# Performance work log

Measured on AMD Instinct MI355X. Metric: run time of the kernel, lower is better.

The kernel has to match this reference:

```python
import jax, jax.numpy as jnp
import numpy as np

B = 32768
T = 1024  # num_time_bins


def setup_inputs() -> dict:
    key = jax.random.key(0)
    k1, k2, k3, k4 = jax.random.split(key, 4)
    hazard_values = jax.random.uniform(k1, (B, T), dtype=jnp.float32)
    labels_Y = jax.random.uniform(k2, (B,), dtype=jnp.float32) * T
    # nn.Linear(T, T): weight [T, T] (out, in), bias [T]
    lim = 1.0 / np.sqrt(T)
    W = jax.random.uniform(k3, (T, T), minval=-lim, maxval=lim, dtype=jnp.float32)
    b = jax.random.uniform(k4, (T,), minval=-lim, maxval=lim, dtype=jnp.float32)
    return {"hazard_values": hazard_values, "labels_Y": labels_Y, "W": W, "b": b}


def reference(hazard_values, labels_Y, W, b):
    # linear + sigmoid + argmax -> per-row truncation position
    logits = hazard_values @ W.T + b                       # [B, T]
    trunc_pos = jnp.argmax(jax.nn.sigmoid(logits), axis=1, keepdims=True)  # [B, 1] int
    # survival curve
    S = jnp.cumprod(1.0 - hazard_values, axis=1)           # [B, T]
    # vectorized truncation decay: for t >= p, multiply by exp(-(t - p))
    t = jnp.arange(T)[None, :]                             # [1, T]
    decay = jnp.where(t >= trunc_pos,
                      jnp.exp(-(t - trunc_pos).astype(S.dtype)),
                      jnp.ones((), S.dtype))
    S = S * decay
    # MSE between argmax position and labels (original prints; we skip prints)
    p = trunc_pos[:, 0].astype(jnp.float32)
    truncation_loss = jnp.mean((p - labels_Y) ** 2)
    return trunc_pos, S, truncation_loss
```

## Files before the change

kernel.cpp:

```cpp
#include <hip/hip_runtime.h>

#define B_ROWS 32768
#define T_BINS 1024

typedef __attribute__((ext_vector_type(8))) _Float16 half8;
typedef __attribute__((ext_vector_type(4))) float floatx4;

__device__ __forceinline__ unsigned long long pack_max(float v, int col) {
    unsigned x = __float_as_uint(v);
    x = (x & 0x80000000u) ? ~x : (x | 0x80000000u);
    return ((unsigned long long)x << 32) | (unsigned)(~col);
}

__device__ __forceinline__ void async16h(const _Float16* g, _Float16* l) {
    __builtin_amdgcn_global_load_lds(
        (const __attribute__((address_space(1))) unsigned int*)g,
        (__attribute__((address_space(3))) unsigned int*)l,
        16, 0, 0);
}

__global__ __launch_bounds__(256) void tof16_kernel(
    const float* __restrict__ src, _Float16* __restrict__ dst, int n4)
{
    int idx = blockIdx.x * 256 + threadIdx.x;
    if (idx >= n4) return;
    float4 x = ((const float4*)src)[idx];
    union { _Float16 h[4]; ushort4 u; } cv;
    cv.h[0] = (_Float16)x.x;
    cv.h[1] = (_Float16)x.y;
    cv.h[2] = (_Float16)x.z;
    cv.h[3] = (_Float16)x.w;
    ((ushort4*)dst)[idx] = cv.u;
}

__global__ __launch_bounds__(256, 3) void mega_kernel(
    const float* __restrict__ A, const _Float16* __restrict__ Wh,
    const float* __restrict__ bias, const float* __restrict__ labels,
    float* __restrict__ out_trunc, float* __restrict__ out_S,
    float* __restrict__ loss_acc)
{
    __shared__ _Float16 sA[2][64 * 32];
    __shared__ _Float16 sW[2][256 * 32];
    __shared__ unsigned long long cand[4][64];
    __shared__ float trunc_s[64];

    const int tid  = threadIdx.x;
    const int lane = tid & 63;
    const int wc   = tid >> 6;
    const int by   = blockIdx.x;

    const int arow  = tid >> 2;
    const int aslot = tid & 3;
    const int sAw   = arow * 32 + ((aslot ^ ((arow ^ (arow >> 2)) & 3)) * 8);
    const float* Abase = A + (size_t)(by * 64 + arow) * T_BINS + aslot * 8;

    const int l2    = lane >> 2;
    const int wksw  = ((lane & 3) ^ ((l2 ^ (l2 >> 2)) & 3)) * 8;
    const int wcol0 = wc * 64 + l2;

    const int l15   = lane & 15;
    const int hi    = lane >> 4;
    const int rslot = ((hi ^ ((l15 ^ (l15 >> 2)) & 3)) * 8);

    float run_best[4][4];
    int   run_col[4][4];
#pragma unroll
    for (int i = 0; i < 4; ++i)
#pragma unroll
        for (int r = 0; r < 4; ++r) { run_best[i][r] = -3.4e38f; run_col[i][r] = 0; }

    {
        float4 f0 = *(const float4*)(Abase);
        float4 f1 = *(const float4*)(Abase + 4);
        half8 hv;
        hv[0] = (_Float16)f0.x; hv[1] = (_Float16)f0.y;
        hv[2] = (_Float16)f0.z; hv[3] = (_Float16)f0.w;
        hv[4] = (_Float16)f1.x; hv[5] = (_Float16)f1.y;
        hv[6] = (_Float16)f1.z; hv[7] = (_Float16)f1.w;
        *(half8*)&sA[0][sAw] = hv;
    }
#pragma unroll
    for (int r = 0; r < 4; ++r)
        async16h(Wh + (size_t)(wcol0 + r * 16) * T_BINS + wksw,
                 &sW[0][wc * 2048 + r * 512]);
    float4 pa0 = *(const float4*)(Abase + 32);
    float4 pa1 = *(const float4*)(Abase + 36);
    asm volatile("s_waitcnt lgkmcnt(0)" ::: "memory");
    __builtin_amdgcn_s_barrier();

    int n = 0;
    for (int bx = 0; bx < 4; ++bx) {
        const int colbase = bx * 256 + wc * 64 + l15;
        float bj[4];
#pragma unroll
        for (int j = 0; j < 4; ++j) bj[j] = bias[colbase + j * 16];

        floatx4 acc[4][4];
#pragma unroll
        for (int i = 0; i < 4; ++i)
#pragma unroll
            for (int j = 0; j < 4; ++j) acc[i][j] = (floatx4){0.f, 0.f, 0.f, 0.f};

        for (int t = 0; t < 32; ++t, ++n) {
            const int cur = n & 1;
            const int nxt = cur ^ 1;
            const int m   = (n + 1) & 127;
            const int bxn = m >> 5;
            const int k0n = (m & 31) * 32;

            const int kq = ((n + 2) & 31) * 32;
            float4 qa0 = *(const float4*)(Abase + kq);
            float4 qa1 = *(const float4*)(Abase + kq + 4);

#pragma unroll
            for (int r = 0; r < 4; ++r)
                async16h(Wh + (size_t)(bxn * 256 + wcol0 + r * 16) * T_BINS + k0n + wksw,
                         &sW[nxt][wc * 2048 + r * 512]);

            {
                half8 hv;
                hv[0] = (_Float16)pa0.x; hv[1] = (_Float16)pa0.y;
                hv[2] = (_Float16)pa0.z; hv[3] = (_Float16)pa0.w;
                hv[4] = (_Float16)pa1.x; hv[5] = (_Float16)pa1.y;
                hv[6] = (_Float16)pa1.z; hv[7] = (_Float16)pa1.w;
                *(half8*)&sA[nxt][sAw] = hv;
            }
            pa0 = qa0; pa1 = qa1;

            asm volatile("s_waitcnt vmcnt(6)" ::: "memory");

            half8 ah[4], whf[4];
#pragma unroll
            for (int i = 0; i < 4; ++i)
                ah[i] = *(const half8*)&sA[cur][(i * 16 + l15) * 32 + rslot];
#pragma unroll
            for (int j = 0; j < 4; ++j)
                whf[j] = *(const half8*)&sW[cur][(wc * 64 + j * 16 + l15) * 32 + rslot];

            __builtin_amdgcn_s_setprio(1);
#pragma unroll
            for (int i = 0; i < 4; ++i)
#pragma unroll
                for (int j = 0; j < 4; ++j)
                    acc[i][j] = __builtin_amdgcn_mfma_f32_16x16x32_f16(ah[i], whf[j], acc[i][j], 0, 0, 0);
            __builtin_amdgcn_s_setprio(0);

            asm volatile("s_waitcnt lgkmcnt(0)" ::: "memory");
            __builtin_amdgcn_s_barrier();
        }

#pragma unroll
        for (int i = 0; i < 4; ++i)
#pragma unroll
            for (int r = 0; r < 4; ++r)
#pragma unroll
                for (int j = 0; j < 4; ++j) {
                    float v = acc[i][j][r] + bj[j];
                    if (v > run_best[i][r]) { run_best[i][r] = v; run_col[i][r] = colbase + j * 16; }
                }
    }

#pragma unroll
    for (int i = 0; i < 4; ++i)
#pragma unroll
        for (int r = 0; r < 4; ++r) {
            float best = run_best[i][r];
            int   bc   = run_col[i][r];
#pragma unroll
            for (int off = 8; off >= 1; off >>= 1) {
                float ov = __shfl_xor(best, off, 64);
                int   oc = __shfl_xor(bc, off, 64);
                if (ov > best || (ov == best && oc < bc)) { best = ov; bc = oc; }
            }
            if ((lane & 15) == 0)
                cand[wc][i * 16 + (lane >> 4) * 4 + r] = pack_max(best, bc);
        }
    __syncthreads();

    if (tid < 64) {
        unsigned long long m01 = cand[0][tid] > cand[1][tid] ? cand[0][tid] : cand[1][tid];
        unsigned long long m23 = cand[2][tid] > cand[3][tid] ? cand[2][tid] : cand[3][tid];
        unsigned long long mm = m01 > m23 ? m01 : m23;
        unsigned col = ~(unsigned)mm;
        float p = (float)col;
        int rowG = by * 64 + tid;
        out_trunc[rowG] = p;
        trunc_s[tid] = p;
        float d = p - labels[rowG];
        float term = d * d * (1.0f / (float)B_ROWS);
#pragma unroll
        for (int off = 32; off >= 1; off >>= 1)
            term += __shfl_down(term, off, 64);
        if (tid == 0) atomicAdd(loss_acc, term);
    }
    __syncthreads();

    for (int rr = 0; rr < 16; ++rr) {
        int row  = wc * 16 + rr;
        int rowG = by * 64 + row;
        const float* Hrow = A + (size_t)rowG * T_BINS + lane * 16;
        float4 h0 = *(const float4*)(Hrow + 0);
        float4 h1 = *(const float4*)(Hrow + 4);
        float4 h2 = *(const float4*)(Hrow + 8);
        float4 h3 = *(const float4*)(Hrow + 12);
        float hv[16] = {h0.x, h0.y, h0.z, h0.w, h1.x, h1.y, h1.z, h1.w,
                        h2.x, h2.y, h2.z, h2.w, h3.x, h3.y, h3.z, h3.w};
        float vprod[16];
        float run = 1.f;
#pragma unroll
        for (int j = 0; j < 16; ++j) { run *= (1.f - hv[j]); vprod[j] = run; }
        float x = run;
#pragma unroll
        for (int off = 1; off < 64; off <<= 1) {
            float o = __shfl_up(x, off, 64);
            if (lane >= off) x *= o;
        }
        float pre = __shfl_up(x, 1, 64);
        if (lane == 0) pre = 1.f;

        int p  = (int)trunc_s[row];
        int t0 = lane * 16;
        float sv[16];
#pragma unroll
        for (int j = 0; j < 16; ++j) {
            float s = pre * vprod[j];
            int t = t0 + j;
            if (t >= p) s *= __expf((float)(p - t));
            sv[j] = s;
        }
        floatx4* Srow = (floatx4*)(out_S + (size_t)rowG * T_BINS + lane * 16);
        floatx4 s0 = {sv[0],  sv[1],  sv[2],  sv[3]};
        floatx4 s1 = {sv[4],  sv[5],  sv[6],  sv[7]};
        floatx4 s2 = {sv[8],  sv[9],  sv[10], sv[11]};
        floatx4 s3 = {sv[12], sv[13], sv[14], sv[15]};
        __builtin_nontemporal_store(s0, Srow + 0);
        __builtin_nontemporal_store(s1, Srow + 1);
        __builtin_nontemporal_store(s2, Srow + 2);
        __builtin_nontemporal_store(s3, Srow + 3);
    }
}

#define BMf 64
#define BKf 16
#define LDSS (BMf + 4)
__global__ __launch_bounds__(256) void gemm_argmax_fp32(
    const float* __restrict__ A, const float* __restrict__ W,
    const float* __restrict__ bias, unsigned long long* __restrict__ rec)
{
    __shared__ float As[BKf][LDSS];
    __shared__ float Ws[BKf][LDSS];
    const int tid = threadIdx.x;
    const int tx = tid & 15, ty = tid >> 4;
    const int bx = blockIdx.x, by = blockIdx.y;
    const int ar = tid >> 2, ak = (tid & 3) << 2;
    const float* Arow = A + (size_t)(by * BMf + ar) * T_BINS + ak;
    const float* Wrow = W + (size_t)(bx * BMf + ar) * T_BINS + ak;
    float acc[4][4];
#pragma unroll
    for (int i = 0; i < 4; ++i)
#pragma unroll
        for (int j = 0; j < 4; ++j) acc[i][j] = 0.f;
    for (int k0 = 0; k0 < T_BINS; k0 += BKf) {
        float4 av = *(const float4*)(Arow + k0);
        float4 wvv = *(const float4*)(Wrow + k0);
        As[ak + 0][ar] = av.x; As[ak + 1][ar] = av.y; As[ak + 2][ar] = av.z; As[ak + 3][ar] = av.w;
        Ws[ak + 0][ar] = wvv.x; Ws[ak + 1][ar] = wvv.y; Ws[ak + 2][ar] = wvv.z; Ws[ak + 3][ar] = wvv.w;
        __syncthreads();
#pragma unroll
        for (int k = 0; k < BKf; ++k) {
            float4 a4 = *(const float4*)&As[k][ty * 4];
            float4 w4 = *(const float4*)&Ws[k][tx * 4];
            float aa[4] = {a4.x, a4.y, a4.z, a4.w};
            float ww[4] = {w4.x, w4.y, w4.z, w4.w};
#pragma unroll
            for (int i = 0; i < 4; ++i)
#pragma unroll
                for (int j = 0; j < 4; ++j) acc[i][j] = fmaf(aa[i], ww[j], acc[i][j]);
        }
        __syncthreads();
    }
    const int colBase = bx * BMf + tx * 4;
    float bv[4];
#pragma unroll
    for (int j = 0; j < 4; ++j) bv[j] = bias[colBase + j];
#pragma unroll
    for (int i = 0; i < 4; ++i) {
        float best = acc[i][0] + bv[0];
        int bc = colBase;
#pragma unroll
        for (int j = 1; j < 4; ++j) {
            float v = acc[i][j] + bv[j];
            if (v > best) { best = v; bc = colBase + j; }
        }
#pragma unroll
        for (int off = 8; off >= 1; off >>= 1) {
            float ov = __shfl_xor(best, off, 64);
            int oc = __shfl_xor(bc, off, 64);
            if (ov > best || (ov == best && oc < bc)) { best = ov; bc = oc; }
        }
        if (tx == 0) atomicMax(&rec[by * BMf + ty * 4 + i], pack_max(best, bc));
    }
}

__global__ __launch_bounds__(256) void finalize_kernel(
    const unsigned long long* __restrict__ rec, const float* __restrict__ labels,
    float* __restrict__ out_trunc, float* __restrict__ loss_acc)
{
    int i = blockIdx.x * 256 + threadIdx.x;
    unsigned col = ~(unsigned)(rec[i] & 0xFFFFFFFFull);
    float p = (float)col;
    out_trunc[i] = p;
    float d = p - labels[i];
    float term = d * d * (1.0f / (float)B_ROWS);
#pragma unroll
    for (int off = 32; off >= 1; off >>= 1)
        term += __shfl_down(term, off, 64);
    __shared__ float partials[4];
    int lane = threadIdx.x & 63, wv = threadIdx.x >> 6;
    if (lane == 0) partials[wv] = term;
    __syncthreads();
    if (threadIdx.x == 0)
        atomicAdd(loss_acc, partials[0] + partials[1] + partials[2] + partials[3]);
}

__global__ __launch_bounds__(256) void scan_kernel_f32(
    const float* __restrict__ H, const float* __restrict__ trunc_f,
    float* __restrict__ Sout)
{
    const int row = blockIdx.x;
    const int tid = threadIdx.x;
    const int lane = tid & 63;
    const int wv = tid >> 6;
    const float4 h = *(const float4*)(H + (size_t)row * T_BINS + tid * 4);
    float l0 = 1.f - h.x;
    float l1 = l0 * (1.f - h.y);
    float l2 = l1 * (1.f - h.z);
    float l3 = l2 * (1.f - h.w);
    float x = l3;
#pragma unroll
    for (int off = 1; off < 64; off <<= 1) {
        float o = __shfl_up(x, off, 64);
        if (lane >= off) x *= o;
    }
    float ex = __shfl_up(x, 1, 64);
    if (lane == 0) ex = 1.f;
    __shared__ float wtot[4];
    if (lane == 63) wtot[wv] = x;
    __syncthreads();
    float wpre = 1.f;
#pragma unroll
    for (int w = 0; w < 3; ++w)
        if (w < wv) wpre *= wtot[w];
    float pre = wpre * ex;
    int p = (int)trunc_f[row];
    int t0 = tid * 4;
    float sv[4] = {pre * l0, pre * l1, pre * l2, pre * l3};
#pragma unroll
    for (int j = 0; j < 4; ++j) {
        int t = t0 + j;
        if (t >= p) sv[j] *= __expf((float)(p - t));
    }
    float4 s4 = {sv[0], sv[1], sv[2], sv[3]};
    *(float4*)(Sout + (size_t)row * T_BINS + tid * 4) = s4;
}

extern "C" void kernel_launch(void* const* d_in, const int* in_sizes, int n_in,
                              void* d_out, int out_size, void* d_ws, size_t ws_size,
                              hipStream_t stream)
{
    const float* hazard = (const float*)d_in[0];
    const float* labels = (const float*)d_in[1];
    const float* W      = (const float*)d_in[2];
    const float* bias   = (const float*)d_in[3];

    float* out       = (float*)d_out;
    float* out_trunc = out;
    float* out_S     = out + B_ROWS;
    float* out_loss  = out + B_ROWS + (size_t)B_ROWS * T_BINS;

    hipMemsetAsync(out_loss, 0, sizeof(float), stream);

    const size_t NW = (size_t)T_BINS * T_BINS;
    if (ws_size >= NW * sizeof(_Float16)) {
        _Float16* Wh = (_Float16*)d_ws;
        tof16_kernel<<<(int)(NW / 4 / 256), 256, 0, stream>>>(W, Wh, (int)(NW / 4));
        mega_kernel<<<B_ROWS / 64, 256, 0, stream>>>(
            hazard, Wh, bias, labels, out_trunc, out_S, out_loss);
    } else {
        unsigned long long* rec = (unsigned long long*)out_S;
        hipMemsetAsync(rec, 0, (size_t)B_ROWS * sizeof(unsigned long long), stream);
        dim3 ggrid(T_BINS / BMf, B_ROWS / BMf);
        gemm_argmax_fp32<<<ggrid, 256, 0, stream>>>(hazard, W, bias, rec);
        finalize_kernel<<<B_ROWS / 256, 256, 0, stream>>>(rec, labels, out_trunc, out_loss);
        scan_kernel_f32<<<B_ROWS, 256, 0, stream>>>(hazard, out_trunc, out_S);
    }
}
```

Baseline: 422.2 us.

## Halve row tile to 32 per block, raise occupancy, drop nontemporal S stores

Shrinks the per-block row tile from 64 to 32, which doubles the grid and halves the MFMA accumulators and A staging per thread, and raises the occupancy hint from 3 to 4 blocks per CU. It also removes the setprio bracketing around the MFMAs and replaces the nontemporal stores of S with ordinary vector stores. The intent is more concurrent waves to hide memory latency. In exchange, each W tile now feeds only 32 rows, so W traffic from L2 to LDS per output doubles and MFMA arithmetic intensity per block drops.

```diff
diff --git a/kernel.cpp b/kernel.cpp
--- a/kernel.cpp
+++ b/kernel.cpp
@@ -2,8 +2,10 @@
 
 #define B_ROWS 32768
 #define T_BINS 1024
+#define M_ROWS 32
 
 typedef __attribute__((ext_vector_type(8))) _Float16 half8;
+typedef __attribute__((ext_vector_type(4))) _Float16 half4v;
 typedef __attribute__((ext_vector_type(4))) float floatx4;
 
 __device__ __forceinline__ unsigned long long pack_max(float v, int col) {
@@ -33,26 +35,27 @@
     ((ushort4*)dst)[idx] = cv.u;
 }
 
-__global__ __launch_bounds__(256, 3) void mega_kernel(
+__global__ __launch_bounds__(256, 4) void mega_kernel(
     const float* __restrict__ A, const _Float16* __restrict__ Wh,
     const float* __restrict__ bias, const float* __restrict__ labels,
     float* __restrict__ out_trunc, float* __restrict__ out_S,
     float* __restrict__ loss_acc)
 {
-    __shared__ _Float16 sA[2][64 * 32];
+    __shared__ _Float16 sA[2][M_ROWS * 32];
     __shared__ _Float16 sW[2][256 * 32];
-    __shared__ unsigned long long cand[4][64];
-    __shared__ float trunc_s[64];
+    __shared__ unsigned long long cand[4][M_ROWS];
+    __shared__ float trunc_s[M_ROWS];
 
     const int tid  = threadIdx.x;
     const int lane = tid & 63;
     const int wc   = tid >> 6;
     const int by   = blockIdx.x;
 
-    const int arow  = tid >> 2;
-    const int aslot = tid & 3;
-    const int sAw   = arow * 32 + ((aslot ^ ((arow ^ (arow >> 2)) & 3)) * 8);
-    const float* Abase = A + (size_t)(by * 64 + arow) * T_BINS + aslot * 8;
+    const int arow = tid >> 3;
+    const int ac4  = tid & 7;
+    const int xr   = (arow ^ (arow >> 2)) & 3;
+    const int sAw  = arow * 32 + (((ac4 >> 1) ^ xr) * 8) + (ac4 & 1) * 4;
+    const float* Abase = A + (size_t)(by * M_ROWS + arow) * T_BINS + ac4 * 4;
 
     const int l2    = lane >> 2;
     const int wksw  = ((lane & 3) ^ ((l2 ^ (l2 >> 2)) & 3)) * 8;
@@ -62,29 +65,25 @@
     const int hi    = lane >> 4;
     const int rslot = ((hi ^ ((l15 ^ (l15 >> 2)) & 3)) * 8);
 
-    float run_best[4][4];
-    int   run_col[4][4];
-#pragma unroll
-    for (int i = 0; i < 4; ++i)
+    float run_best[2][4];
+    int   run_col[2][4];
+#pragma unroll
+    for (int i = 0; i < 2; ++i)
 #pragma unroll
         for (int r = 0; r < 4; ++r) { run_best[i][r] = -3.4e38f; run_col[i][r] = 0; }
 
     {
         float4 f0 = *(const float4*)(Abase);
-        float4 f1 = *(const float4*)(Abase + 4);
-        half8 hv;
+        half4v hv;
         hv[0] = (_Float16)f0.x; hv[1] = (_Float16)f0.y;
         hv[2] = (_Float16)f0.z; hv[3] = (_Float16)f0.w;
-        hv[4] = (_Float16)f1.x; hv[5] = (_Float16)f1.y;
-        hv[6] = (_Float16)f1.z; hv[7] = (_Float16)f1.w;
-        *(half8*)&sA[0][sAw] = hv;
+        *(half4v*)&sA[0][sAw] = hv;
     }
 #pragma unroll
     for (int r = 0; r < 4; ++r)
         async16h(Wh + (size_t)(wcol0 + r * 16) * T_BINS + wksw,
                  &sW[0][wc * 2048 + r * 512]);
-    float4 pa0 = *(const float4*)(Abase + 32);
-    float4 pa1 = *(const float4*)(Abase + 36);
+    float4 pa = *(const float4*)(Abase + 32);
     asm volatile("s_waitcnt lgkmcnt(0)" ::: "memory");
     __builtin_amdgcn_s_barrier();
 
@@ -95,9 +94,9 @@
 #pragma unroll
         for (int j = 0; j < 4; ++j) bj[j] = bias[colbase + j * 16];
 
-        floatx4 acc[4][4];
-#pragma unroll
-        for (int i = 0; i < 4; ++i)
+        floatx4 acc[2][4];
+#pragma unroll
+        for (int i = 0; i < 2; ++i)
 #pragma unroll
             for (int j = 0; j < 4; ++j) acc[i][j] = (floatx4){0.f, 0.f, 0.f, 0.f};
 
@@ -109,8 +108,7 @@
             const int k0n = (m & 31) * 32;
 
             const int kq = ((n + 2) & 31) * 32;
-            float4 qa0 = *(const float4*)(Abase + kq);
-            float4 qa1 = *(const float4*)(Abase + kq + 4);
+            float4 qa = *(const float4*)(Abase + kq);
 
 #pragma unroll
             for (int r = 0; r < 4; ++r)
@@ -118,39 +116,35 @@
                          &sW[nxt][wc * 2048 + r * 512]);
 
             {
-                half8 hv;
-                hv[0] = (_Float16)pa0.x; hv[1] = (_Float16)pa0.y;
-                hv[2] = (_Float16)pa0.z; hv[3] = (_Float16)pa0.w;
-                hv[4] = (_Float16)pa1.x; hv[5] = (_Float16)pa1.y;
-                hv[6] = (_Float16)pa1.z; hv[7] = (_Float16)pa1.w;
-                *(half8*)&sA[nxt][sAw] = hv;
+                half4v hv;
+                hv[0] = (_Float16)pa.x; hv[1] = (_Float16)pa.y;
+                hv[2] = (_Float16)pa.z; hv[3] = (_Float16)pa.w;
+                *(half4v*)&sA[nxt][sAw] = hv;
             }
-            pa0 = qa0; pa1 = qa1;
-
-            asm volatile("s_waitcnt vmcnt(6)" ::: "memory");
-
-            half8 ah[4], whf[4];
-#pragma unroll
-            for (int i = 0; i < 4; ++i)
+            pa = qa;
+
+            asm volatile("s_waitcnt vmcnt(5)" ::: "memory");
+
+            half8 ah[2], whf[4];
+#pragma unroll
+            for (int i = 0; i < 2; ++i)
                 ah[i] = *(const half8*)&sA[cur][(i * 16 + l15) * 32 + rslot];
 #pragma unroll
             for (int j = 0; j < 4; ++j)
                 whf[j] = *(const half8*)&sW[cur][(wc * 64 + j * 16 + l15) * 32 + rslot];
 
-            __builtin_amdgcn_s_setprio(1);
-#pragma unroll
-            for (int i = 0; i < 4; ++i)
+#pragma unroll
+            for (int i = 0; i < 2; ++i)
 #pragma unroll
                 for (int j = 0; j < 4; ++j)
                     acc[i][j] = __builtin_amdgcn_mfma_f32_16x16x32_f16(ah[i], whf[j], acc[i][j], 0, 0, 0);
-            __builtin_amdgcn_s_setprio(0);
 
             asm volatile("s_waitcnt lgkmcnt(0)" ::: "memory");
             __builtin_amdgcn_s_barrier();
         }
 
 #pragma unroll
-        for (int i = 0; i < 4; ++i)
+        for (int i = 0; i < 2; ++i)
 #pragma unroll
             for (int r = 0; r < 4; ++r)
 #pragma unroll
@@ -161,7 +155,7 @@
     }
 
 #pragma unroll
-    for (int i = 0; i < 4; ++i)
+    for (int i = 0; i < 2; ++i)
 #pragma unroll
         for (int r = 0; r < 4; ++r) {
             float best = run_best[i][r];
@@ -177,27 +171,27 @@
         }
     __syncthreads();
 
-    if (tid < 64) {
+    if (tid < M_ROWS) {
         unsigned long long m01 = cand[0][tid] > cand[1][tid] ? cand[0][tid] : cand[1][tid];
         unsigned long long m23 = cand[2][tid] > cand[3][tid] ? cand[2][tid] : cand[3][tid];
         unsigned long long mm = m01 > m23 ? m01 : m23;
         unsigned col = ~(unsigned)mm;
         float p = (float)col;
-        int rowG = by * 64 + tid;
+        int rowG = by * M_ROWS + tid;
         out_trunc[rowG] = p;
         trunc_s[tid] = p;
         float d = p - labels[rowG];
         float term = d * d * (1.0f / (float)B_ROWS);
 #pragma unroll
-        for (int off = 32; off >= 1; off >>= 1)
+        for (int off = 16; off >= 1; off >>= 1)
             term += __shfl_down(term, off, 64);
         if (tid == 0) atomicAdd(loss_acc, term);
     }
     __syncthreads();
 
-    for (int rr = 0; rr < 16; ++rr) {
-        int row  = wc * 16 + rr;
-        int rowG = by * 64 + row;
+    for (int rr = 0; rr < 8; ++rr) {
+        int row  = wc * 8 + rr;
+        int rowG = by * M_ROWS + row;
         const float* Hrow = A + (size_t)rowG * T_BINS + lane * 16;
         float4 h0 = *(const float4*)(Hrow + 0);
         float4 h1 = *(const float4*)(Hrow + 4);
@@ -228,15 +222,11 @@
             if (t >= p) s *= __expf((float)(p - t));
             sv[j] = s;
         }
-        floatx4* Srow = (floatx4*)(out_S + (size_t)rowG * T_BINS + lane * 16);
-        floatx4 s0 = {sv[0],  sv[1],  sv[2],  sv[3]};
-        floatx4 s1 = {sv[4],  sv[5],  sv[6],  sv[7]};
-        floatx4 s2 = {sv[8],  sv[9],  sv[10], sv[11]};
-        floatx4 s3 = {sv[12], sv[13], sv[14], sv[15]};
-        __builtin_nontemporal_store(s0, Srow + 0);
-        __builtin_nontemporal_store(s1, Srow + 1);
-        __builtin_nontemporal_store(s2, Srow + 2);
-        __builtin_nontemporal_store(s3, Srow + 3);
+        float* Srow = out_S + (size_t)rowG * T_BINS + lane * 16;
+        *(float4*)(Srow + 0)  = (float4){sv[0],  sv[1],  sv[2],  sv[3]};
+        *(float4*)(Srow + 4)  = (float4){sv[4],  sv[5],  sv[6],  sv[7]};
+        *(float4*)(Srow + 8)  = (float4){sv[8],  sv[9],  sv[10], sv[11]};
+        *(float4*)(Srow + 12) = (float4){sv[12], sv[13], sv[14], sv[15]};
     }
 }
 
@@ -384,7 +374,7 @@
     if (ws_size >= NW * sizeof(_Float16)) {
         _Float16* Wh = (_Float16*)d_ws;
         tof16_kernel<<<(int)(NW / 4 / 256), 256, 0, stream>>>(W, Wh, (int)(NW / 4));
-        mega_kernel<<<B_ROWS / 64, 256, 0, stream>>>(
+        mega_kernel<<<B_ROWS / M_ROWS, 256, 0, stream>>>(
             hazard, Wh, bias, labels, out_trunc, out_S, out_loss);
     } else {
         unsigned long long* rec = (unsigned long long*)out_S;
```

Measured after the change: 461.1 us. +9.2%, slower.
